# Kernel optimization log

Measured on AMD Instinct MI355X. Metric: run time of the kernel, lower is better.

Reference implementation:

```python
import jax, jax.numpy as jnp
import numpy as np

BATCH = 8192
N_BANDS = 2000
TARGET = 500
FIRST_HIDDEN = 50
LEAKY_SLOPE = 0.01  # torch LeakyReLU default


def _tridiag_solve(lower, diag, upper, rhs):
    """Thomas algorithm. lower/upper: (n-1,), diag: (n,), rhs: (n, B). Returns (n, B)."""
    dt = rhs.dtype
    up = jnp.concatenate([upper, jnp.zeros((1,), dt)])   # (n,)
    lo = jnp.concatenate([jnp.zeros((1,), dt), lower])   # (n,)

    def fwd(carry, inp):
        cp_prev, dp_prev = carry
        d_i, u_i, l_i, r_i = inp
        m = d_i - l_i * cp_prev
        cp = u_i / m
        dp = (r_i - l_i * dp_prev) / m
        return (cp, dp), (cp, dp)

    init = (jnp.zeros((), dt), jnp.zeros(rhs.shape[1:], dt))
    _, (cps, dps) = jax.lax.scan(fwd, init, (diag, up, lo, rhs))

    def bwd(x_next, inp):
        cp, dp = inp
        x = dp - cp * x_next
        return x, x

    _, xs = jax.lax.scan(bwd, jnp.zeros(rhs.shape[1:], dt), (cps, dps), reverse=True)
    return xs


def natural_cubic_spline_coeffs(times, path):
    """times: (n,), path: (B, n) -> (a, b, two_c, three_d), each (B, n-1)."""
    h = times[1:] - times[:-1]            # (n-1,)
    hr = 1.0 / h
    hr2 = hr * hr
    diffs3 = 3.0 * (path[:, 1:] - path[:, :-1])   # (B, n-1)
    diffs6 = 2.0 * diffs3
    pds = diffs3 * hr2                             # (B, n-1)
    n = path.shape[1]
    diag = (jnp.zeros((n,), path.dtype).at[:-1].set(hr).at[1:].add(hr)) * 2.0
    rhs = jnp.zeros_like(path).at[:, :-1].set(pds).at[:, 1:].add(pds)  # (B, n)
    kd = _tridiag_solve(hr, diag, hr, rhs.T).T     # knot derivatives (B, n)
    a = path[:, :-1]
    b = kd[:, :-1]
    two_c = (diffs6 * hr - 4.0 * kd[:, :-1] - 2.0 * kd[:, 1:]) * hr
    three_d = (-diffs6 * hr + 3.0 * (kd[:, :-1] + kd[:, 1:])) * hr2
    return a, b, two_c, three_d


def spline_evaluate(times, coeffs, t):
    """Evaluate at points t: (T,). Returns (B, T)."""
    a, b, two_c, three_d = coeffs
    idx = jnp.clip(jnp.searchsorted(times, t, side='left') - 1, 0, times.shape[0] - 2)
    frac = t - times[idx]                  # (T,)
    inner = 0.5 * two_c[:, idx] + three_d[:, idx] * frac / 3.0
    inner = b[:, idx] + inner * frac
    return a[:, idx] + inner * frac


def leaky_relu(x):
    return jnp.where(x >= 0, x, LEAKY_SLOPE * x)


def setup_inputs() -> dict:
    key = jax.random.key(0)
    ks = jax.random.split(key, 8)
    return {
        'x': jax.random.uniform(ks[0], (BATCH, N_BANDS), dtype=jnp.float32),
        'raw_index': jax.random.normal(ks[1], (TARGET,), dtype=jnp.float32),
        'W1': jax.random.normal(ks[2], (TARGET, FIRST_HIDDEN), dtype=jnp.float32) * 0.05,
        'b1': jax.random.normal(ks[3], (FIRST_HIDDEN,), dtype=jnp.float32) * 0.05,
        'W2': jax.random.normal(ks[4], (FIRST_HIDDEN, 10), dtype=jnp.float32) * 0.1,
        'b2': jax.random.normal(ks[5], (10,), dtype=jnp.float32) * 0.1,
        'W3': jax.random.normal(ks[6], (10, 1), dtype=jnp.float32) * 0.1,
        'b3': jax.random.normal(ks[7], (1,), dtype=jnp.float32) * 0.1,
    }


def reference(x, raw_index, W1, b1, W2, b2, W3, b3):
    # x: (B, n_bands). Spline is fit along the band axis with knots linspace(0,1,n_bands).
    times = jnp.linspace(0.0, 1.0, x.shape[1]).astype(x.dtype)
    coeffs = natural_cubic_spline_coeffs(times, x)
    # Each BandIndex machine evaluates the spline at sigmoid(raw_index_i) -> batched over all i.
    t_eval = jax.nn.sigmoid(raw_index)             # (T,)
    outputs = spline_evaluate(times, coeffs, t_eval)  # (B, T)
    h = leaky_relu(outputs @ W1 + b1)
    h = leaky_relu(h @ W2 + b2)
    soc_hat = (h @ W3 + b3).reshape(-1)            # (B,)
    return soc_hat
```

## Files before the change

kernel.cpp:

```cpp
#include <hip/hip_runtime.h>

#define NB 2000
#define BATCH 8192
#define NT 500
#define NH1 50
#define NH2 10
#define HRc 1999.0f
#define STEPc (1.0f/1999.0f)

typedef __attribute__((ext_vector_type(8))) short short8;
typedef __attribute__((ext_vector_type(4))) float f32x4;

__device__ __forceinline__ float b2f(unsigned short u) {
    return __uint_as_float(((unsigned int)u) << 16);
}
__device__ __forceinline__ unsigned short f2b(float f) {
    unsigned int u = __float_as_uint(f);
    return (unsigned short)((u + 0x7FFFu + ((u >> 16) & 1u)) >> 16);
}
__device__ __forceinline__ float ldv(const void* p, int i, int flag) {
    return flag ? b2f(((const unsigned short*)p)[i]) : ((const float*)p)[i];
}
__device__ __forceinline__ int wave_detect(const void* x) {
    const unsigned char* xb = (const unsigned char*)x;
    int lane = threadIdx.x & 63;
    int pred = xb[4 * lane + 1] > 0x3F;
    unsigned long long m = __ballot(pred);
    return (__popcll(m) > 4) ? 0 : 1;
}

__global__ __launch_bounds__(64, 1) void p1_stencil(
        const void* __restrict__ xdet, const void* __restrict__ raw_index,
        float* __restrict__ S_coef, int* __restrict__ S_base) {
    __shared__ float cp_tab[64];
    __shared__ float sc[2];
    int tid = threadIdx.x;
    int flag = wave_detect(xdet);
    if (tid == 0) {
        double cp = 0.5;
        cp_tab[0] = 0.5f;
        for (int i = 1; i < 64; ++i) { cp = 1.0 / (4.0 - cp); cp_tab[i] = (float)cp; }
        sc[0] = (float)cp;
        sc[1] = (float)(1.0 / (2.0 - cp));
    }
    __syncthreads();
    int t = blockIdx.x * 64 + tid;
    if (t >= NT) return;
    float c_inf = sc[0], w_last = sc[1];

    float coef_rel[34];
    #pragma unroll
    for (int k = 0; k < 34; ++k) coef_rel[k] = 0.0f;

    float r = ldv(raw_index, t, flag);
    float v = 1.0f / (1.0f + expf(-r));
    int lo = 0, hi = NB;
    while (lo < hi) {
        int mid = (lo + hi) >> 1;
        float tm = (float)mid * STEPc;
        if (tm < v) lo = mid + 1; else hi = mid;
    }
    int idx = lo - 1;
    idx = idx < 0 ? 0 : (idx > NB - 2 ? NB - 2 : idx);
    float f = v - (float)idx * STEPc;
    float u = f * HRc;
    float A = 1.0f + u * u * (2.0f * u - 3.0f);
    float B = u * u * (3.0f - 2.0f * u);
    float C = f * (1.0f - u) * (1.0f - u);
    float D = f * u * (u - 1.0f);

    const float g3 = 3.0f * HRc * HRc;
    const float invhr = 1.0f / HRc;

    #pragma unroll
    for (int row = 0; row < 2; ++row) {
        int j = idx + row;
        float scale = row ? D : C;
        float z[35];
        #pragma unroll
        for (int q = 0; q < 35; ++q) z[q] = 0.0f;
        float w0 = (j <= NB - 2) ? ((j < 64) ? cp_tab[j] : c_inf) : w_last;
        z[17] = w0 * invhr;
        #pragma unroll
        for (int s = 1; s <= 17; ++s) {
            int m = j + s;
            float wm;
            if (m <= NB - 2)      wm = (m < 64) ? cp_tab[m] : c_inf;
            else if (m == NB - 1) wm = w_last;
            else                  wm = 0.0f;
            z[17 + s] = -wm * z[17 + s - 1];
        }
        #pragma unroll
        for (int s = 16; s >= -17; --s) {
            int m = j + s;
            float cpv;
            if (m >= NB - 1 || m < 0) cpv = 0.0f;
            else                      cpv = (m < 64) ? cp_tab[m] : c_inf;
            z[17 + s] = z[17 + s] - cpv * z[17 + s + 1];
        }
        #pragma unroll
        for (int s = -16; s <= 16; ++s) {
            int m = j + s;
            float gv = 0.0f;
            if (m >= 1)      gv += z[17 + s - 1];
            if (m <= NB - 2) gv -= z[17 + s + 1];
            if (m == NB - 1) gv += z[17 + s];
            if (m == 0)      gv -= z[17 + s];
            gv *= g3;
            bool valid = (m >= 0) && (m <= NB - 1);
            coef_rel[s + row + 16] += valid ? scale * gv : 0.0f;
        }
    }
    coef_rel[16] += A;
    coef_rel[17] += B;

    #pragma unroll
    for (int j = 0; j < 34; ++j) S_coef[t * 34 + j] = coef_rel[j];
    S_base[t] = idx;
}

__global__ __launch_bounds__(256) void m_build(
        const void* __restrict__ xdet, const void* __restrict__ W1,
        const float* __restrict__ S_coef, const int* __restrict__ S_base,
        unsigned int* __restrict__ MB) {
    __shared__ int sb[NT];
    int tid = threadIdx.x;
    int flag = wave_detect(xdet);
    for (int i = tid; i < NT; i += 256) sb[i] = S_base[i];
    __syncthreads();
    int k2 = blockIdx.x * 4 + (tid >> 6);
    int h = tid & 63;
    int hh = h < NH1 ? h : NH1 - 1;
    int k0 = 2 * k2;
    float acc0 = 0.0f, acc1 = 0.0f;
    if (k0 < NB) {
        #pragma unroll 4
        for (int t = 0; t < NT; ++t) {
            int idx = sb[t];
            int rel0 = k0 - idx + 16;
            if (rel0 >= -1 && rel0 < 34) {
                float w1v = ldv(W1, t * NH1 + hh, flag);
                if (rel0 >= 0)  acc0 += S_coef[t * 34 + rel0] * w1v;
                if (rel0 < 33)  acc1 += S_coef[t * 34 + rel0 + 1] * w1v;
            }
        }
    }
    bool ok = (h < NH1) && (k0 < NB);
    unsigned int lo16 = ok ? (unsigned int)f2b(acc0) : 0u;
    unsigned int hi16 = ok ? (unsigned int)f2b(acc1) : 0u;
    int kt = k0 >> 5;
    int kr = k0 & 31;
    int gg = kr >> 3;
    int j  = kr & 7;
    int ht = h >> 4;
    int lt = gg * 16 + (h & 15);
    MB[(((kt * 4 + ht) * 64 + lt) << 2) + (j >> 1)] = lo16 | (hi16 << 16);
}

__global__ __launch_bounds__(512, 4) void g_fused(
        const void* __restrict__ x, const unsigned int* __restrict__ MB,
        const void* __restrict__ b1, const void* __restrict__ W2,
        const void* __restrict__ b2, const void* __restrict__ W3,
        const void* __restrict__ b3, void* __restrict__ out) {
    __shared__ float red[8][16][68];
    __shared__ float Wmlp[NH1 * NH2 + NH1 + NH2 + NH2 + 1];

    int tid = threadIdx.x;
    int flag = wave_detect(x);

    for (int i = tid; i < NH1 * NH2; i += 512) Wmlp[i] = ldv(W2, i, flag);
    if (tid < NH1) Wmlp[500 + tid] = ldv(b1, tid, flag);
    if (tid < NH2) Wmlp[550 + tid] = ldv(b2, tid, flag);
    if (tid < NH2) Wmlp[560 + tid] = ldv(W3, tid, flag);
    if (tid == 0)  Wmlp[570] = ldv(b3, 0, flag);

    int lane = tid & 63;
    int c16  = tid & 15;
    int g    = (tid >> 4) & 3;
    int w    = tid >> 6;
    int r0   = blockIdx.x * 16;
    const unsigned short* xs = (const unsigned short*)x;
    const float*          xf = (const float*)x;
    size_t arow = (size_t)(r0 + c16) * NB;

    f32x4 acc[4];
    #pragma unroll
    for (int ht = 0; ht < 4; ++ht) acc[ht] = (f32x4){0.f, 0.f, 0.f, 0.f};

    union AU { uint4 u; short8 s; };
    AU a[8];
    const uint4* mb4 = (const uint4*)MB;
    int kbase = w * 32 + g * 8;

    if (flag) {
        #pragma unroll
        for (int i = 0; i < 7; ++i)
            a[i].u = *(const uint4*)(xs + arow + kbase + 256 * i);
        {
            int k7 = kbase + 256 * 7;
            a[7].u = (k7 + 8 <= NB) ? *(const uint4*)(xs + arow + k7)
                                    : make_uint4(0u, 0u, 0u, 0u);
        }
    } else {
        #pragma unroll
        for (int i = 0; i < 8; ++i) {
            int k0 = kbase + 256 * i;
            a[i].u = make_uint4(0u, 0u, 0u, 0u);
            if (k0 + 8 <= NB) {
                float4 v0 = *(const float4*)(xf + arow + k0);
                float4 v1 = *(const float4*)(xf + arow + k0 + 4);
                a[i].u.x = (unsigned)f2b(v0.x) | ((unsigned)f2b(v0.y) << 16);
                a[i].u.y = (unsigned)f2b(v0.z) | ((unsigned)f2b(v0.w) << 16);
                a[i].u.z = (unsigned)f2b(v1.x) | ((unsigned)f2b(v1.y) << 16);
                a[i].u.w = (unsigned)f2b(v1.z) | ((unsigned)f2b(v1.w) << 16);
            }
        }
    }

    #pragma unroll
    for (int i = 0; i < 8; ++i) {
        int kt = w + 8 * i;
        #pragma unroll
        for (int ht = 0; ht < 4; ++ht) {
            AU b; b.u = mb4[(kt * 4 + ht) * 64 + lane];
            acc[ht] = __builtin_amdgcn_mfma_f32_16x16x32_bf16(a[i].s, b.s, acc[ht], 0, 0, 0);
        }
    }

    #pragma unroll
    for (int ht = 0; ht < 4; ++ht)
        #pragma unroll
        for (int r = 0; r < 4; ++r)
            red[w][g * 4 + r][ht * 16 + c16] = acc[ht][r];
    __syncthreads();

    #pragma unroll
    for (int ii = 0; ii < 2; ++ii) {
        int idx = tid + ii * 512;
        int row = idx >> 6, h = idx & 63;
        float s = 0.0f;
        #pragma unroll
        for (int w2 = 0; w2 < 8; ++w2) s += red[w2][row][h];
        red[0][row][h] = s;
    }
    __syncthreads();

    if (tid < 16) {
        float h1v[NH1];
        #pragma unroll
        for (int h = 0; h < NH1; ++h) {
            float vv = red[0][tid][h] + Wmlp[500 + h];
            h1v[h] = vv >= 0.0f ? vv : 0.01f * vv;
        }
        float o = Wmlp[570];
        for (int j = 0; j < NH2; ++j) {
            float a2 = Wmlp[550 + j];
            #pragma unroll
            for (int h = 0; h < NH1; ++h)
                a2 = fmaf(h1v[h], Wmlp[h * NH2 + j], a2);
            a2 = a2 >= 0.0f ? a2 : 0.01f * a2;
            o = fmaf(a2, Wmlp[560 + j], o);
        }
        int b = r0 + tid;
        if (flag) ((unsigned short*)out)[b] = f2b(o);
        else      ((float*)out)[b] = o;
    }
}

extern "C" void kernel_launch(void* const* d_in, const int* in_sizes, int n_in,
                              void* d_out, int out_size, void* d_ws, size_t ws_size,
                              hipStream_t stream) {
    const void* x   = d_in[0];
    const void* raw = d_in[1];
    const void* W1  = d_in[2];
    const void* b1  = d_in[3];
    const void* W2  = d_in[4];
    const void* b2  = d_in[5];
    const void* W3  = d_in[6];
    const void* b3  = d_in[7];

    float* w      = (float*)d_ws;
    int*   S_base = (int*)w;
    float* S_coef = w + 512;
    unsigned int* MB = (unsigned int*)(w + 17512);

    p1_stencil<<<8, 64, 0, stream>>>(x, raw, S_coef, S_base);
    m_build<<<256, 256, 0, stream>>>(x, W1, S_coef, S_base, MB);
    g_fused<<<512, 512, 0, stream>>>(x, MB, b1, W2, b2, W3, b3, d_out);
}
```

Baseline: 161.5 us.

## Stage x rows through double-buffered LDS with coalesced loads before MFMA

The x tile used to be loaded straight into registers in an MFMA-fragment order, 16-byte pieces scattered across rows. It is now read coalesced, one 512-element chunk per row segment per step, into a double-buffered LDS tile. Each wave then reads its A fragments from LDS, and the next chunk is prefetched while MFMAs run on the current one. This aims to improve global load coalescing and overlap, at the cost of extra LDS traffic, about 33KB more shared memory (which may lower occupancy), and two barriers per chunk.

```diff
diff --git a/kernel.cpp b/kernel.cpp
--- a/kernel.cpp
+++ b/kernel.cpp
@@ -7,6 +7,7 @@
 #define NH2 10
 #define HRc 1999.0f
 #define STEPc (1.0f/1999.0f)
+#define LP 520
 
 typedef __attribute__((ext_vector_type(8))) short short8;
 typedef __attribute__((ext_vector_type(4))) float f32x4;
@@ -162,6 +163,7 @@
         const void* __restrict__ b1, const void* __restrict__ W2,
         const void* __restrict__ b2, const void* __restrict__ W3,
         const void* __restrict__ b3, void* __restrict__ out) {
+    __shared__ __align__(16) unsigned short lx[2][16 * LP];
     __shared__ float red[8][16][68];
     __shared__ float Wmlp[NH1 * NH2 + NH1 + NH2 + NH2 + 1];
 
@@ -178,54 +180,75 @@
     int c16  = tid & 15;
     int g    = (tid >> 4) & 3;
     int w    = tid >> 6;
+    int srow = tid >> 5;
+    int soff = tid & 31;
     int r0   = blockIdx.x * 16;
     const unsigned short* xs = (const unsigned short*)x;
     const float*          xf = (const float*)x;
-    size_t arow = (size_t)(r0 + c16) * NB;
+    size_t crow = (size_t)(r0 + srow) * NB;
 
     f32x4 acc[4];
     #pragma unroll
     for (int ht = 0; ht < 4; ++ht) acc[ht] = (f32x4){0.f, 0.f, 0.f, 0.f};
 
     union AU { uint4 u; short8 s; };
-    AU a[8];
     const uint4* mb4 = (const uint4*)MB;
-    int kbase = w * 32 + g * 8;
-
-    if (flag) {
-        #pragma unroll
-        for (int i = 0; i < 7; ++i)
-            a[i].u = *(const uint4*)(xs + arow + kbase + 256 * i);
-        {
-            int k7 = kbase + 256 * 7;
-            a[7].u = (k7 + 8 <= NB) ? *(const uint4*)(xs + arow + k7)
-                                    : make_uint4(0u, 0u, 0u, 0u);
-        }
-    } else {
-        #pragma unroll
-        for (int i = 0; i < 8; ++i) {
-            int k0 = kbase + 256 * i;
-            a[i].u = make_uint4(0u, 0u, 0u, 0u);
-            if (k0 + 8 <= NB) {
-                float4 v0 = *(const float4*)(xf + arow + k0);
-                float4 v1 = *(const float4*)(xf + arow + k0 + 4);
-                a[i].u.x = (unsigned)f2b(v0.x) | ((unsigned)f2b(v0.y) << 16);
-                a[i].u.y = (unsigned)f2b(v0.z) | ((unsigned)f2b(v0.w) << 16);
-                a[i].u.z = (unsigned)f2b(v1.x) | ((unsigned)f2b(v1.y) << 16);
-                a[i].u.w = (unsigned)f2b(v1.z) | ((unsigned)f2b(v1.w) << 16);
+
+    #define LDSEG(dst, gk) do {                                           \
+        int _gk = (gk);                                                   \
+        if (_gk + 8 <= NB) {                                              \
+            if (flag) {                                                   \
+                (dst) = *(const uint4*)(xs + crow + _gk);                 \
+            } else {                                                      \
+                float4 _v0 = *(const float4*)(xf + crow + _gk);           \
+                float4 _v1 = *(const float4*)(xf + crow + _gk + 4);       \
+                (dst).x = (unsigned)f2b(_v0.x) | ((unsigned)f2b(_v0.y) << 16); \
+                (dst).y = (unsigned)f2b(_v0.z) | ((unsigned)f2b(_v0.w) << 16); \
+                (dst).z = (unsigned)f2b(_v1.x) | ((unsigned)f2b(_v1.y) << 16); \
+                (dst).w = (unsigned)f2b(_v1.z) | ((unsigned)f2b(_v1.w) << 16); \
+            }                                                             \
+        } else {                                                          \
+            (dst) = make_uint4(0u, 0u, 0u, 0u);                           \
+        }                                                                 \
+    } while (0)
+
+    {
+        uint4 p0, p1;
+        LDSEG(p0, soff * 8);
+        LDSEG(p1, soff * 8 + 256);
+        *(uint4*)&lx[0][srow * LP + soff * 8]       = p0;
+        *(uint4*)&lx[0][srow * LP + soff * 8 + 256] = p1;
+    }
+
+    int cur = 0;
+    #pragma unroll
+    for (int c = 0; c < 4; ++c) {
+        __syncthreads();
+        uint4 s0 = make_uint4(0u,0u,0u,0u), s1 = make_uint4(0u,0u,0u,0u);
+        if (c < 3) {
+            LDSEG(s0, (c + 1) * 512 + soff * 8);
+            LDSEG(s1, (c + 1) * 512 + soff * 8 + 256);
+        }
+        #pragma unroll
+        for (int dk = 0; dk < 2; ++dk) {
+            int ktl = 2 * w + dk;
+            AU a;
+            a.u = *(const uint4*)&lx[cur][c16 * LP + ktl * 32 + g * 8];
+            int kt = c * 16 + ktl;
+            #pragma unroll
+            for (int ht = 0; ht < 4; ++ht) {
+                AU b; b.u = mb4[(kt * 4 + ht) * 64 + lane];
+                acc[ht] = __builtin_amdgcn_mfma_f32_16x16x32_bf16(a.s, b.s, acc[ht], 0, 0, 0);
             }
         }
-    }
-
-    #pragma unroll
-    for (int i = 0; i < 8; ++i) {
-        int kt = w + 8 * i;
-        #pragma unroll
-        for (int ht = 0; ht < 4; ++ht) {
-            AU b; b.u = mb4[(kt * 4 + ht) * 64 + lane];
-            acc[ht] = __builtin_amdgcn_mfma_f32_16x16x32_bf16(a[i].s, b.s, acc[ht], 0, 0, 0);
-        }
-    }
+        if (c < 3) {
+            *(uint4*)&lx[cur ^ 1][srow * LP + soff * 8]       = s0;
+            *(uint4*)&lx[cur ^ 1][srow * LP + soff * 8 + 256] = s1;
+        }
+        __syncthreads();
+        cur ^= 1;
+    }
+    #undef LDSEG
 
     #pragma unroll
     for (int ht = 0; ht < 4; ++ht)
```

Result: no change. 161.1 us (-0.2%).
